# Performance work log

Hardware: AMD Instinct MI355X
Metric: run time of the kernel (lower is better)

Reference implementation:

```python
import jax, jax.numpy as jnp
import numpy as np

N_NODES = 100000
N_EDGES = 1600000
N_GRAPHS = 1024
F_NODE = 16
F_EDGE = 8
F_GRAPH = 10
F_OUT = 1
H = 64
EPS = 1e-7  # GENConv eps
T = 1.0     # GENConv softmax temperature (learn_t=False default)


def _lin_init(key, fi, fo):
    kw, kb = jax.random.split(key)
    s = 1.0 / np.sqrt(fi)
    W = jax.random.uniform(kw, (fi, fo), jnp.float32, -s, s)
    b = jax.random.uniform(kb, (fo,), jnp.float32, -s, s)
    return W, b


def setup_inputs() -> dict:
    key = jax.random.key(0)
    ks = jax.random.split(key, 24)
    inp = {
        'x': jax.random.normal(ks[0], (N_NODES, F_NODE), jnp.float32),
        'edge_attr': jax.random.normal(ks[1], (N_EDGES, F_EDGE), jnp.float32),
        'graph_attr': jax.random.normal(ks[2], (N_GRAPHS, F_GRAPH), jnp.float32),
        'edge_index': jax.random.randint(ks[3], (2, N_EDGES), 0, N_NODES),
        'batch': jnp.sort(jax.random.randint(ks[4], (N_NODES,), 0, N_GRAPHS)),
    }
    inp['node_W'], inp['node_b'] = _lin_init(ks[5], F_NODE, H)
    inp['edge_W'], inp['edge_b'] = _lin_init(ks[6], F_EDGE, H)
    # three GENConv MLPs: Linear(H,2H) -> BN(identity @eval) -> ReLU -> Linear(2H,H)
    for i, k1, k2 in ((1, ks[7], ks[8]), (2, ks[9], ks[10]), (3, ks[11], ks[12])):
        inp[f'c{i}_W1'], inp[f'c{i}_b1'] = _lin_init(k1, H, 2 * H)
        inp[f'c{i}_W2'], inp[f'c{i}_b2'] = _lin_init(k2, 2 * H, H)
    inp['d1_W'], inp['d1_b'] = _lin_init(ks[13], H + F_GRAPH, 32)
    inp['d2_W'], inp['d2_b'] = _lin_init(ks[14], 32, 32)
    inp['out_W'], inp['out_b'] = _lin_init(ks[15], 32, F_OUT)
    return inp


def _genconv(h, src, dst, ea, W1, b1, W2, b2):
    # message: relu(x_j + edge_attr) + eps   [E, H]
    msg = jax.nn.relu(h[src] + ea) + EPS
    # per-destination, per-feature segment softmax (aggr='softmax', t=1)
    m = jax.ops.segment_max(msg * T, dst, num_segments=N_NODES)   # [N, H]
    e = jnp.exp(msg * T - m[dst])                                  # [E, H]
    denom = jax.ops.segment_sum(e, dst, num_segments=N_NODES)     # [N, H]
    alpha = e / jnp.maximum(denom[dst], 1e-16)
    agg = jax.ops.segment_sum(msg * alpha, dst, num_segments=N_NODES)
    out = h + agg  # root add
    # MLP (BatchNorm is identity in eval with default stats)
    hid = jax.nn.relu(out @ W1 + b1)
    return hid @ W2 + b2


def reference(x, edge_attr, graph_attr, node_W, node_b, edge_W, edge_b,
              c1_W1, c1_b1, c1_W2, c1_b2,
              c2_W1, c2_b1, c2_W2, c2_b2,
              c3_W1, c3_b1, c3_W2, c3_b2,
              d1_W, d1_b, d2_W, d2_b, out_W, out_b,
              edge_index, batch):
    src, dst = edge_index[0], edge_index[1]
    h = x @ node_W + node_b
    ea = edge_attr @ edge_W + edge_b
    h = jax.nn.relu(_genconv(h, src, dst, ea, c1_W1, c1_b1, c1_W2, c1_b2))
    h = jax.nn.relu(_genconv(h, src, dst, ea, c2_W1, c2_b1, c2_W2, c2_b2))
    h = jax.nn.relu(_genconv(h, src, dst, ea, c3_W1, c3_b1, c3_W2, c3_b2))
    # global mean pool over graphs
    sums = jax.ops.segment_sum(h, batch, num_segments=N_GRAPHS)          # [G, H]
    cnt = jax.ops.segment_sum(jnp.ones((h.shape[0],), h.dtype), batch, num_segments=N_GRAPHS)
    pooled = sums / jnp.maximum(cnt, 1.0)[:, None]
    g = jnp.concatenate([pooled, graph_attr], axis=1)                    # [G, H+F_GRAPH]
    g = jax.nn.relu(g @ d1_W + d1_b)   # dropout = identity at eval
    g = jax.nn.relu(g @ d2_W + d2_b)
    return jax.nn.sigmoid(g @ out_W + out_b)                             # [G, 1]
```

## Files before the change

### kernel.cpp

```cpp
#include <hip/hip_runtime.h>
#include <hip/hip_bf16.h>

#define N_NODES 100000
#define N_EDGES 1600000
#define N_GRAPHS 1024
#define F_NODE 16
#define F_EDGE 8
#define F_GRAPH 10
#define HD 64
#define HD2 128
#define GEN_EPS 1e-7f
#define SCAN_NBLK ((N_NODES + 255) / 256)

typedef unsigned short u16;
typedef unsigned int u32;
typedef __attribute__((ext_vector_type(8))) short short8;
typedef __attribute__((ext_vector_type(4))) float floatx4;

__device__ __forceinline__ u16 f2bf(float x) {
    u32 u = __float_as_uint(x);
    return (u16)((u + 0x7FFFu + ((u >> 16) & 1u)) >> 16);
}
__device__ __forceinline__ float bf2f(u16 u) {
    return __uint_as_float(((u32)u) << 16);
}
__device__ __forceinline__ float u2f(unsigned int u) {
    return __uint_as_float(u);
}

__global__ void __launch_bounds__(256) k_node_embed(
        const float* __restrict__ x, const float* __restrict__ W,
        const float* __restrict__ b, float* __restrict__ h,
        u16* __restrict__ hb) {
    __shared__ float sW[F_NODE * HD];
    __shared__ float sb[HD];
    for (int i = threadIdx.x; i < F_NODE * HD; i += 256) sW[i] = W[i];
    if (threadIdx.x < HD) sb[threadIdx.x] = b[threadIdx.x];
    __syncthreads();
    int t = blockIdx.x * 256 + threadIdx.x;
    if (t >= N_NODES * HD) return;
    int n = t >> 6, f = t & 63;
    const float* xr = x + (size_t)n * F_NODE;
    float acc = sb[f];
#pragma unroll
    for (int k = 0; k < F_NODE; k++) acc += xr[k] * sW[k * HD + f];
    h[t] = acc;
    hb[t] = f2bf(acc);
}

__global__ void __launch_bounds__(256) k_hist(
        const int* __restrict__ dst, int* __restrict__ deg,
        int* __restrict__ rank) {
    int e = blockIdx.x * 256 + threadIdx.x;
    if (e >= N_EDGES) return;
    rank[e] = atomicAdd(&deg[dst[e]], 1);
}

__global__ void __launch_bounds__(256) k_scan1(
        const int* __restrict__ deg, int* __restrict__ bsum) {
    __shared__ int red[256];
    int t = threadIdx.x;
    int g = blockIdx.x * 256 + t;
    red[t] = (g < N_NODES) ? deg[g] : 0;
    __syncthreads();
    for (int s = 128; s > 0; s >>= 1) {
        if (t < s) red[t] += red[t + s];
        __syncthreads();
    }
    if (t == 0) bsum[blockIdx.x] = red[0];
}

__global__ void __launch_bounds__(512) k_scan2(
        const int* __restrict__ bsum, int* __restrict__ bpre) {
    __shared__ int sh[512];
    int t = threadIdx.x;
    int v = (t < SCAN_NBLK) ? bsum[t] : 0;
    sh[t] = v;
    __syncthreads();
    for (int d = 1; d < 512; d <<= 1) {
        int u = (t >= d) ? sh[t - d] : 0;
        __syncthreads();
        sh[t] += u;
        __syncthreads();
    }
    if (t < SCAN_NBLK) bpre[t] = sh[t] - v;
}

__global__ void __launch_bounds__(256) k_scan3(
        const int* __restrict__ deg, const int* __restrict__ bpre,
        int* __restrict__ off) {
    __shared__ int sh[256];
    int t = threadIdx.x;
    int g = blockIdx.x * 256 + t;
    int v = (g < N_NODES) ? deg[g] : 0;
    sh[t] = v;
    __syncthreads();
    for (int d = 1; d < 256; d <<= 1) {
        int u = (t >= d) ? sh[t - d] : 0;
        __syncthreads();
        sh[t] += u;
        __syncthreads();
    }
    int incl = sh[t];
    int base = bpre[blockIdx.x];
    if (g < N_NODES) off[g] = base + incl - v;
    if (g == N_NODES - 1) off[N_NODES] = base + incl;
}

__global__ void __launch_bounds__(256) k_scatter(
        const int* __restrict__ src, const int* __restrict__ dst,
        const int* __restrict__ rank, const int* __restrict__ off,
        const float* __restrict__ eattr,
        unsigned int* __restrict__ rec, int* __restrict__ srcs) {
    int e = blockIdx.x * 256 + threadIdx.x;
    if (e >= N_EDGES) return;
    const uint4* ap = reinterpret_cast<const uint4*>(eattr + (size_t)e * F_EDGE);
    uint4 a0 = ap[0], a1 = ap[1];
    int pos = off[dst[e]] + rank[e];
    uint4* op = reinterpret_cast<uint4*>(rec + (size_t)pos * 8);
    op[0] = a0;
    op[1] = a1;
    srcs[pos] = src[e];
}

__global__ void __launch_bounds__(256) k_gen_agg(
        const float* __restrict__ h, const u16* __restrict__ hb,
        const int* __restrict__ off,
        const unsigned int* __restrict__ rec,
        const int* __restrict__ srcs,
        const float* __restrict__ eW, const float* __restrict__ eb,
        float* __restrict__ outb) {
    int f = threadIdx.x & 63;
    float w[F_EDGE];
#pragma unroll
    for (int k = 0; k < F_EDGE; k++) w[k] = eW[k * HD + f];
    float bf = eb[f];
    int wave0 = blockIdx.x * 4 + (threadIdx.x >> 6);
    const int NW = gridDim.x * 4;
    for (int n0 = wave0; n0 < N_NODES; n0 += NW) {
        int n = __builtin_amdgcn_readfirstlane(n0);
        int beg = off[n], end = off[n + 1];
        size_t idx = (size_t)n * HD + f;
        float hroot = h[idx];
        float den = 0.f, nm = 0.f;
        int i = beg;
        for (; i + 8 <= end; i += 8) {
            uint4 q0[8], q1[8];
#pragma unroll
            for (int u = 0; u < 8; u++) {
                const uint4* rp = reinterpret_cast<const uint4*>(
                    rec + (size_t)(i + u) * 8);
                q0[u] = rp[0];
                q1[u] = rp[1];
            }
            int s[8];
#pragma unroll
            for (int u = 0; u < 8; u++) s[u] = srcs[i + u];
            float hv[8];
#pragma unroll
            for (int u = 0; u < 8; u++) hv[u] = bf2f(hb[(size_t)s[u] * HD + f]);
#pragma unroll
            for (int u = 0; u < 8; u++) {
                float ea = bf + u2f(q0[u].x) * w[0] + u2f(q0[u].y) * w[1]
                              + u2f(q0[u].z) * w[2] + u2f(q0[u].w) * w[3]
                              + u2f(q1[u].x) * w[4] + u2f(q1[u].y) * w[5]
                              + u2f(q1[u].z) * w[6] + u2f(q1[u].w) * w[7];
                float r = fmaxf(hv[u] + ea, 0.f);
                float ev = __expf(r);
                den += ev;
                nm += r * ev;
            }
        }
        for (; i < end; i++) {
            const uint4* rp = reinterpret_cast<const uint4*>(rec + (size_t)i * 8);
            uint4 q0 = rp[0], q1 = rp[1];
            int s = srcs[i];
            float hv = bf2f(hb[(size_t)s * HD + f]);
            float ea = bf + u2f(q0.x) * w[0] + u2f(q0.y) * w[1]
                          + u2f(q0.z) * w[2] + u2f(q0.w) * w[3]
                          + u2f(q1.x) * w[4] + u2f(q1.y) * w[5]
                          + u2f(q1.z) * w[6] + u2f(q1.w) * w[7];
            float r = fmaxf(hv + ea, 0.f);
            float ev = __expf(r);
            den += ev;
            nm += r * ev;
        }
        float agg = (end > beg) ? (nm / fmaxf(den, 1e-16f) + GEN_EPS) : 0.f;
        outb[idx] = hroot + agg;
    }
}

__global__ void __launch_bounds__(256) k_mlp(
        const float* __restrict__ inb,
        const float* __restrict__ W1, const float* __restrict__ b1,
        const float* __restrict__ W2, const float* __restrict__ b2,
        float* __restrict__ hout, u16* __restrict__ hbout) {
    __shared__ u16 wB1[HD2][HD + 8];
    __shared__ u16 wB2[HD][HD2 + 8];
    __shared__ u16 sHid[64][HD2 + 8];
    __shared__ float sb1[HD2];
    __shared__ float sb2[HD];
    int tid = threadIdx.x;
    for (int i = tid; i < HD * HD2; i += 256) {
        int f = i >> 7, j = i & 127;
        wB1[j][f] = f2bf(W1[i]);
    }
    for (int i = tid; i < HD2 * HD; i += 256) {
        int j = i >> 6, c = i & 63;
        wB2[c][j] = f2bf(W2[i]);
    }
    if (tid < HD2) sb1[tid] = b1[tid];
    if (tid < HD) sb2[tid] = b2[tid];
    __syncthreads();
    int wid = tid >> 6, lane = tid & 63;
    int quad = lane >> 4, lm = lane & 15;
    int n0 = blockIdx.x * 64 + wid * 16;
    bool active = (n0 < N_NODES);
    if (active) {
        int node = n0 + lm;
        short8 a[2];
        const float* ar = inb + (size_t)node * HD;
#pragma unroll
        for (int kk = 0; kk < 2; kk++) {
            const float4* p = reinterpret_cast<const float4*>(ar + kk * 32 + quad * 8);
            float4 v0 = p[0], v1 = p[1];
            short8 t;
            t[0] = (short)f2bf(v0.x); t[1] = (short)f2bf(v0.y);
            t[2] = (short)f2bf(v0.z); t[3] = (short)f2bf(v0.w);
            t[4] = (short)f2bf(v1.x); t[5] = (short)f2bf(v1.y);
            t[6] = (short)f2bf(v1.z); t[7] = (short)f2bf(v1.w);
            a[kk] = t;
        }
#pragma unroll
        for (int jt = 0; jt < 8; jt++) {
            int jb = jt * 16;
            float bias = sb1[jb + lm];
            floatx4 acc = {bias, bias, bias, bias};
#pragma unroll
            for (int kk = 0; kk < 2; kk++) {
                const short8* bp = reinterpret_cast<const short8*>(
                    &wB1[jb + lm][kk * 32 + quad * 8]);
                acc = __builtin_amdgcn_mfma_f32_16x16x32_bf16(a[kk], *bp, acc, 0, 0, 0);
            }
#pragma unroll
            for (int r = 0; r < 4; r++) {
                int lr = wid * 16 + quad * 4 + r;
                sHid[lr][jb + lm] = f2bf(fmaxf(acc[r], 0.f));
            }
        }
    }
    __syncthreads();
    if (active) {
        short8 a2[4];
#pragma unroll
        for (int kk = 0; kk < 4; kk++)
            a2[kk] = *reinterpret_cast<const short8*>(
                &sHid[wid * 16 + lm][kk * 32 + quad * 8]);
#pragma unroll
        for (int ct = 0; ct < 4; ct++) {
            int cb = ct * 16;
            float bias = sb2[cb + lm];
            floatx4 acc = {bias, bias, bias, bias};
#pragma unroll
            for (int kk = 0; kk < 4; kk++) {
                const short8* bp = reinterpret_cast<const short8*>(
                    &wB2[cb + lm][kk * 32 + quad * 8]);
                acc = __builtin_amdgcn_mfma_f32_16x16x32_bf16(a2[kk], *bp, acc, 0, 0, 0);
            }
#pragma unroll
            for (int r = 0; r < 4; r++) {
                int orow = n0 + quad * 4 + r;
                float o = fmaxf(acc[r], 0.f);
                hout[(size_t)orow * HD + cb + lm] = o;
                hbout[(size_t)orow * HD + cb + lm] = f2bf(o);
            }
        }
    }
}

__global__ void __launch_bounds__(256) k_pool(
        const float* __restrict__ h, const int* __restrict__ batch,
        float* __restrict__ pooled) {
    int g = blockIdx.x * 4 + (threadIdx.x >> 6);
    if (g >= N_GRAPHS) return;
    int f = threadIdx.x & 63;
    int lo = 0, hi = N_NODES;
    while (lo < hi) {
        int mid = (lo + hi) >> 1;
        if (batch[mid] < g) lo = mid + 1; else hi = mid;
    }
    int b = lo;
    int lo2 = b, hi2 = N_NODES;
    while (lo2 < hi2) {
        int mid = (lo2 + hi2) >> 1;
        if (batch[mid] < g + 1) lo2 = mid + 1; else hi2 = mid;
    }
    int e = lo2;
    float s = 0.f;
    for (int n = b; n < e; n++) s += h[(size_t)n * HD + f];
    float cnt = fmaxf((float)(e - b), 1.f);
    pooled[(size_t)g * HD + f] = s / cnt;
}

__global__ void __launch_bounds__(64) k_head(
        const float* __restrict__ pooled, const float* __restrict__ gattr,
        const float* __restrict__ d1W, const float* __restrict__ d1b,
        const float* __restrict__ d2W, const float* __restrict__ d2b,
        const float* __restrict__ oW, const float* __restrict__ ob,
        float* __restrict__ out) {
    int g = blockIdx.x;
    __shared__ float si[HD + F_GRAPH];
    __shared__ float s1[32], s2[32];
    int t = threadIdx.x;
    if (t < HD) si[t] = pooled[(size_t)g * HD + t];
    if (t < F_GRAPH) si[HD + t] = gattr[(size_t)g * F_GRAPH + t];
    __syncthreads();
    if (t < 32) {
        float acc = d1b[t];
        for (int i = 0; i < HD + F_GRAPH; i++) acc += si[i] * d1W[i * 32 + t];
        s1[t] = fmaxf(acc, 0.f);
    }
    __syncthreads();
    if (t < 32) {
        float acc = d2b[t];
        for (int i = 0; i < 32; i++) acc += s1[i] * d2W[i * 32 + t];
        s2[t] = fmaxf(acc, 0.f);
    }
    __syncthreads();
    if (t == 0) {
        float acc = ob[0];
        for (int i = 0; i < 32; i++) acc += s2[i] * oW[i];
        out[g] = 1.f / (1.f + __expf(-acc));
    }
}

extern "C" void kernel_launch(void* const* d_in, const int* in_sizes, int n_in,
                              void* d_out, int out_size, void* d_ws, size_t ws_size,
                              hipStream_t stream) {
    const float* x     = (const float*)d_in[0];
    const float* eattr = (const float*)d_in[1];
    const float* gattr = (const float*)d_in[2];
    const int*   eidx  = (const int*)d_in[3];
    const int*   batch = (const int*)d_in[4];
    const float* nodeW = (const float*)d_in[5];
    const float* nodeb = (const float*)d_in[6];
    const float* edgeW = (const float*)d_in[7];
    const float* edgeb = (const float*)d_in[8];
    const float* cW1[3] = {(const float*)d_in[9],  (const float*)d_in[13], (const float*)d_in[17]};
    const float* cb1[3] = {(const float*)d_in[10], (const float*)d_in[14], (const float*)d_in[18]};
    const float* cW2[3] = {(const float*)d_in[11], (const float*)d_in[15], (const float*)d_in[19]};
    const float* cb2[3] = {(const float*)d_in[12], (const float*)d_in[16], (const float*)d_in[20]};
    const float* d1W = (const float*)d_in[21];
    const float* d1b = (const float*)d_in[22];
    const float* d2W = (const float*)d_in[23];
    const float* d2b = (const float*)d_in[24];
    const float* oW  = (const float*)d_in[25];
    const float* ob  = (const float*)d_in[26];

    const int* src = eidx;
    const int* dst = eidx + N_EDGES;

    char* p = (char*)d_ws;
    float* h      = (float*)p; p += (size_t)N_NODES * HD * 4;
    float* outb   = (float*)p; p += (size_t)N_NODES * HD * 4;
    int*   srcs   = (int*)p;   p += (size_t)N_EDGES * 4;
    unsigned int* rec = (unsigned int*)p; p += (size_t)N_EDGES * F_EDGE * 4;
    u16*   hb     = (u16*)p;   p += (size_t)N_NODES * HD * 2;
    float* pooled = (float*)p; p += (size_t)N_GRAPHS * HD * 4;
    int*   off    = (int*)p;   p += (size_t)(N_NODES + 1) * 4;
    int*   deg    = (int*)p;   p += (size_t)N_NODES * 4;
    int*   rank   = (int*)p;   p += (size_t)N_EDGES * 4;
    int*   bsum   = (int*)p;   p += (size_t)(SCAN_NBLK + 1) * 4;
    int*   bpre   = (int*)p;   p += (size_t)(SCAN_NBLK + 1) * 4;

    const int EB = (N_EDGES + 255) / 256;
    const int NBM = (N_NODES + 63) / 64;

    k_node_embed<<<(N_NODES * HD + 255) / 256, 256, 0, stream>>>(x, nodeW, nodeb, h, hb);

    hipMemsetAsync(deg, 0, (size_t)N_NODES * 4, stream);
    k_hist<<<EB, 256, 0, stream>>>(dst, deg, rank);
    k_scan1<<<SCAN_NBLK, 256, 0, stream>>>(deg, bsum);
    k_scan2<<<1, 512, 0, stream>>>(bsum, bpre);
    k_scan3<<<SCAN_NBLK, 256, 0, stream>>>(deg, bpre, off);
    k_scatter<<<EB, 256, 0, stream>>>(src, dst, rank, off, eattr, rec, srcs);

    for (int l = 0; l < 3; l++) {
        k_gen_agg<<<2048, 256, 0, stream>>>(
            h, hb, off, rec, srcs, edgeW, edgeb, outb);
        k_mlp<<<NBM, 256, 0, stream>>>(outb, cW1[l], cb1[l], cW2[l], cb2[l], h, hb);
    }

    k_pool<<<(N_GRAPHS + 3) / 4, 256, 0, stream>>>(h, batch, pooled);
    k_head<<<N_GRAPHS, 64, 0, stream>>>(pooled, gattr,
                                        d1W, d1b, d2W, d2b, oW, ob,
                                        (float*)d_out);
}
```

Baseline: 716.7 us.

## Load edge records cooperatively per wave and broadcast via readlane; fuse hist with embed

In the aggregation kernel, each wave now loads 8 edge records (64 floats) with one coalesced per-lane load, plus 8 source indices, and broadcasts values with readlane. Previously every lane redundantly loaded the full 32-byte records. The next chunk is prefetched one step ahead, and the remainder loop is folded into a predicated main loop. The histogram and node-embedding kernels are merged into one launch, and edge buffers are padded by 8 entries so the over-read on the last chunk stays in bounds. In exchange, readlane adds scalar instruction overhead, and partial chunks run under per-edge predication.

Result: slower. 870.4 us (+21.4%).

```diff
diff --git a/kernel.cpp b/kernel.cpp
--- a/kernel.cpp
+++ b/kernel.cpp
@@ -11,6 +11,8 @@
 #define HD2 128
 #define GEN_EPS 1e-7f
 #define SCAN_NBLK ((N_NODES + 255) / 256)
+#define EB_BLK ((N_EDGES + 255) / 256)
+#define EMB_BLK ((N_NODES * HD + 255) / 256)
 
 typedef unsigned short u16;
 typedef unsigned int u32;
@@ -27,17 +29,28 @@
 __device__ __forceinline__ float u2f(unsigned int u) {
     return __uint_as_float(u);
 }
-
-__global__ void __launch_bounds__(256) k_node_embed(
+__device__ __forceinline__ float rlanef(u32 v, int l) {
+    return __uint_as_float((u32)__builtin_amdgcn_readlane((int)v, l));
+}
+
+__global__ void __launch_bounds__(256) k_front(
+        const int* __restrict__ dst, int* __restrict__ deg,
+        int* __restrict__ rank,
         const float* __restrict__ x, const float* __restrict__ W,
         const float* __restrict__ b, float* __restrict__ h,
         u16* __restrict__ hb) {
     __shared__ float sW[F_NODE * HD];
     __shared__ float sb[HD];
+    int bid = blockIdx.x;
+    if (bid < EB_BLK) {
+        int e = bid * 256 + threadIdx.x;
+        if (e < N_EDGES) rank[e] = atomicAdd(&deg[dst[e]], 1);
+        return;
+    }
     for (int i = threadIdx.x; i < F_NODE * HD; i += 256) sW[i] = W[i];
     if (threadIdx.x < HD) sb[threadIdx.x] = b[threadIdx.x];
     __syncthreads();
-    int t = blockIdx.x * 256 + threadIdx.x;
+    int t = (bid - EB_BLK) * 256 + threadIdx.x;
     if (t >= N_NODES * HD) return;
     int n = t >> 6, f = t & 63;
     const float* xr = x + (size_t)n * F_NODE;
@@ -46,14 +59,6 @@
     for (int k = 0; k < F_NODE; k++) acc += xr[k] * sW[k * HD + f];
     h[t] = acc;
     hb[t] = f2bf(acc);
-}
-
-__global__ void __launch_bounds__(256) k_hist(
-        const int* __restrict__ dst, int* __restrict__ deg,
-        int* __restrict__ rank) {
-    int e = blockIdx.x * 256 + threadIdx.x;
-    if (e >= N_EDGES) return;
-    rank[e] = atomicAdd(&deg[dst[e]], 1);
 }
 
 __global__ void __launch_bounds__(256) k_scan1(
@@ -130,7 +135,8 @@
         const int* __restrict__ srcs,
         const float* __restrict__ eW, const float* __restrict__ eb,
         float* __restrict__ outb) {
-    int f = threadIdx.x & 63;
+    int lane = threadIdx.x & 63;
+    int f = lane;
     float w[F_EDGE];
 #pragma unroll
     for (int k = 0; k < F_EDGE; k++) w[k] = eW[k * HD + f];
@@ -143,47 +149,44 @@
         size_t idx = (size_t)n * HD + f;
         float hroot = h[idx];
         float den = 0.f, nm = 0.f;
-        int i = beg;
-        for (; i + 8 <= end; i += 8) {
-            uint4 q0[8], q1[8];
-#pragma unroll
-            for (int u = 0; u < 8; u++) {
-                const uint4* rp = reinterpret_cast<const uint4*>(
-                    rec + (size_t)(i + u) * 8);
-                q0[u] = rp[0];
-                q1[u] = rp[1];
-            }
-            int s[8];
-#pragma unroll
-            for (int u = 0; u < 8; u++) s[u] = srcs[i + u];
-            float hv[8];
-#pragma unroll
-            for (int u = 0; u < 8; u++) hv[u] = bf2f(hb[(size_t)s[u] * HD + f]);
-#pragma unroll
-            for (int u = 0; u < 8; u++) {
-                float ea = bf + u2f(q0[u].x) * w[0] + u2f(q0[u].y) * w[1]
-                              + u2f(q0[u].z) * w[2] + u2f(q0[u].w) * w[3]
-                              + u2f(q1[u].x) * w[4] + u2f(q1[u].y) * w[5]
-                              + u2f(q1[u].z) * w[6] + u2f(q1[u].w) * w[7];
-                float r = fmaxf(hv[u] + ea, 0.f);
-                float ev = __expf(r);
-                den += ev;
-                nm += r * ev;
-            }
-        }
-        for (; i < end; i++) {
-            const uint4* rp = reinterpret_cast<const uint4*>(rec + (size_t)i * 8);
-            uint4 q0 = rp[0], q1 = rp[1];
-            int s = srcs[i];
-            float hv = bf2f(hb[(size_t)s * HD + f]);
-            float ea = bf + u2f(q0.x) * w[0] + u2f(q0.y) * w[1]
-                          + u2f(q0.z) * w[2] + u2f(q0.w) * w[3]
-                          + u2f(q1.x) * w[4] + u2f(q1.y) * w[5]
-                          + u2f(q1.z) * w[6] + u2f(q1.w) * w[7];
-            float r = fmaxf(hv + ea, 0.f);
-            float ev = __expf(r);
-            den += ev;
-            nm += r * ev;
+        if (beg < end) {
+            u32 bl = rec[(size_t)beg * 8 + lane];
+            int sv = srcs[beg + (lane & 7)];
+            for (int i = beg; i < end; i += 8) {
+                u32 blN = 0; int svN = 0;
+                int inx = i + 8;
+                if (inx < end) {
+                    blN = rec[(size_t)inx * 8 + lane];
+                    svN = srcs[inx + (lane & 7)];
+                }
+                float hv[8];
+#pragma unroll
+                for (int u = 0; u < 8; u++) {
+                    if (i + u < end) {
+                        int s = __builtin_amdgcn_readlane(sv, u);
+                        hv[u] = bf2f(hb[(size_t)s * HD + f]);
+                    }
+                }
+#pragma unroll
+                for (int u = 0; u < 8; u++) {
+                    if (i + u < end) {
+                        float ea = bf
+                            + rlanef(bl, 8 * u + 0) * w[0]
+                            + rlanef(bl, 8 * u + 1) * w[1]
+                            + rlanef(bl, 8 * u + 2) * w[2]
+                            + rlanef(bl, 8 * u + 3) * w[3]
+                            + rlanef(bl, 8 * u + 4) * w[4]
+                            + rlanef(bl, 8 * u + 5) * w[5]
+                            + rlanef(bl, 8 * u + 6) * w[6]
+                            + rlanef(bl, 8 * u + 7) * w[7];
+                        float r = fmaxf(hv[u] + ea, 0.f);
+                        float ev = __expf(r);
+                        den += ev;
+                        nm += r * ev;
+                    }
+                }
+                bl = blN; sv = svN;
+            }
         }
         float agg = (end > beg) ? (nm / fmaxf(den, 1e-16f) + GEN_EPS) : 0.f;
         outb[idx] = hroot + agg;
@@ -202,8 +205,8 @@
     __shared__ float sb2[HD];
     int tid = threadIdx.x;
     for (int i = tid; i < HD * HD2; i += 256) {
-        int f = i >> 7, j = i & 127;
-        wB1[j][f] = f2bf(W1[i]);
+        int ff = i >> 7, j = i & 127;
+        wB1[j][ff] = f2bf(W1[i]);
     }
     for (int i = tid; i < HD2 * HD; i += 256) {
         int j = i >> 6, c = i & 63;
@@ -363,8 +366,8 @@
     char* p = (char*)d_ws;
     float* h      = (float*)p; p += (size_t)N_NODES * HD * 4;
     float* outb   = (float*)p; p += (size_t)N_NODES * HD * 4;
-    int*   srcs   = (int*)p;   p += (size_t)N_EDGES * 4;
-    unsigned int* rec = (unsigned int*)p; p += (size_t)N_EDGES * F_EDGE * 4;
+    int*   srcs   = (int*)p;   p += (size_t)(N_EDGES + 8) * 4;
+    unsigned int* rec = (unsigned int*)p; p += (size_t)(N_EDGES + 8) * F_EDGE * 4;
     u16*   hb     = (u16*)p;   p += (size_t)N_NODES * HD * 2;
     float* pooled = (float*)p; p += (size_t)N_GRAPHS * HD * 4;
     int*   off    = (int*)p;   p += (size_t)(N_NODES + 1) * 4;
@@ -373,17 +376,15 @@
     int*   bsum   = (int*)p;   p += (size_t)(SCAN_NBLK + 1) * 4;
     int*   bpre   = (int*)p;   p += (size_t)(SCAN_NBLK + 1) * 4;
 
-    const int EB = (N_EDGES + 255) / 256;
     const int NBM = (N_NODES + 63) / 64;
 
-    k_node_embed<<<(N_NODES * HD + 255) / 256, 256, 0, stream>>>(x, nodeW, nodeb, h, hb);
-
     hipMemsetAsync(deg, 0, (size_t)N_NODES * 4, stream);
-    k_hist<<<EB, 256, 0, stream>>>(dst, deg, rank);
+    k_front<<<EB_BLK + EMB_BLK, 256, 0, stream>>>(dst, deg, rank,
+                                                  x, nodeW, nodeb, h, hb);
     k_scan1<<<SCAN_NBLK, 256, 0, stream>>>(deg, bsum);
     k_scan2<<<1, 512, 0, stream>>>(bsum, bpre);
     k_scan3<<<SCAN_NBLK, 256, 0, stream>>>(deg, bpre, off);
-    k_scatter<<<EB, 256, 0, stream>>>(src, dst, rank, off, eattr, rec, srcs);
+    k_scatter<<<EB_BLK, 256, 0, stream>>>(src, dst, rank, off, eattr, rec, srcs);
 
     for (int l = 0; l < 3; l++) {
         k_gen_agg<<<2048, 256, 0, stream>>>(
```

## Assign contiguous node chunks per wave and prefetch neighbor indices via lane broadcast

Applied to the files above, without the earlier changes.

Each wave now handles a contiguous range of KPW nodes instead of a strided set. It loads that range's offsets into lanes once and reads the per-node CSR bounds with readlane. Source indices for the next node are loaded one node ahead and broadcast lane-by-lane, so up to 32 neighbor feature gathers are issued before the edge-record loads. This removes dependent scalar loads of off and srcs from the inner loop. In exchange it adds padding of srcs and rec, a tail loop for nodes with degree above 32, and more register pressure from the 32-entry hv array.

Result: slower. 1.037 ms (+44.6%).

```diff
diff --git a/kernel.cpp b/kernel.cpp
--- a/kernel.cpp
+++ b/kernel.cpp
@@ -11,6 +11,9 @@
 #define HD2 128
 #define GEN_EPS 1e-7f
 #define SCAN_NBLK ((N_NODES + 255) / 256)
+#define AGG_BLK 2048
+#define NWAVES (AGG_BLK * 4)
+#define KPW ((N_NODES + NWAVES - 1) / NWAVES)
 
 typedef unsigned short u16;
 typedef unsigned int u32;
@@ -130,63 +133,94 @@
         const int* __restrict__ srcs,
         const float* __restrict__ eW, const float* __restrict__ eb,
         float* __restrict__ outb) {
-    int f = threadIdx.x & 63;
+    int lane = threadIdx.x & 63;
+    int f = lane;
     float w[F_EDGE];
 #pragma unroll
     for (int k = 0; k < F_EDGE; k++) w[k] = eW[k * HD + f];
     float bf = eb[f];
-    int wave0 = blockIdx.x * 4 + (threadIdx.x >> 6);
-    const int NW = gridDim.x * 4;
-    for (int n0 = wave0; n0 < N_NODES; n0 += NW) {
-        int n = __builtin_amdgcn_readfirstlane(n0);
-        int beg = off[n], end = off[n + 1];
-        size_t idx = (size_t)n * HD + f;
-        float hroot = h[idx];
+    int wv = blockIdx.x * 4 + (threadIdx.x >> 6);
+    int nbeg = wv * KPW;
+    if (nbeg >= N_NODES) return;
+    int nend = nbeg + KPW;
+    if (nend > N_NODES) nend = N_NODES;
+    int cnt = nend - nbeg;
+    int oidx = nbeg + lane;
+    if (oidx > N_NODES) oidx = N_NODES;
+    int offv = off[oidx];
+    int beg = __builtin_amdgcn_readlane(offv, 0);
+    int end = __builtin_amdgcn_readlane(offv, 1);
+    int sv = srcs[beg + lane];
+    float hroot = h[(size_t)nbeg * HD + f];
+    for (int j = 0; j < cnt; j++) {
+        int n = nbeg + j;
+        int deg = end - beg;
+        float hv[32];
+#pragma unroll
+        for (int g8 = 0; g8 < 4; g8++) {
+            if (g8 * 8 < deg) {
+#pragma unroll
+                for (int u = 0; u < 8; u++) {
+                    int s = __builtin_amdgcn_readlane(sv, g8 * 8 + u);
+                    hv[g8 * 8 + u] = bf2f(hb[(size_t)s * HD + f]);
+                }
+            }
+        }
+        int endN = 0, svN = 0;
+        float hrootN = 0.f;
+        if (j + 1 < cnt) {
+            endN = __builtin_amdgcn_readlane(offv, j + 2);
+            svN = srcs[end + lane];
+            hrootN = h[(size_t)(n + 1) * HD + f];
+        }
         float den = 0.f, nm = 0.f;
-        int i = beg;
-        for (; i + 8 <= end; i += 8) {
-            uint4 q0[8], q1[8];
-#pragma unroll
-            for (int u = 0; u < 8; u++) {
-                const uint4* rp = reinterpret_cast<const uint4*>(
-                    rec + (size_t)(i + u) * 8);
-                q0[u] = rp[0];
-                q1[u] = rp[1];
-            }
-            int s[8];
-#pragma unroll
-            for (int u = 0; u < 8; u++) s[u] = srcs[i + u];
-            float hv[8];
-#pragma unroll
-            for (int u = 0; u < 8; u++) hv[u] = bf2f(hb[(size_t)s[u] * HD + f]);
-#pragma unroll
-            for (int u = 0; u < 8; u++) {
-                float ea = bf + u2f(q0[u].x) * w[0] + u2f(q0[u].y) * w[1]
-                              + u2f(q0[u].z) * w[2] + u2f(q0[u].w) * w[3]
-                              + u2f(q1[u].x) * w[4] + u2f(q1[u].y) * w[5]
-                              + u2f(q1[u].z) * w[6] + u2f(q1[u].w) * w[7];
-                float r = fmaxf(hv[u] + ea, 0.f);
-                float ev = __expf(r);
-                den += ev;
-                nm += r * ev;
-            }
-        }
-        for (; i < end; i++) {
+#pragma unroll
+        for (int c = 0; c < 4; c++) {
+            int i0 = beg + c * 8;
+            if (i0 < end) {
+                uint4 q0[8], q1[8];
+#pragma unroll
+                for (int u = 0; u < 8; u++) {
+                    const uint4* rp = reinterpret_cast<const uint4*>(
+                        rec + (size_t)(i0 + u) * 8);
+                    q0[u] = rp[0];
+                    q1[u] = rp[1];
+                }
+#pragma unroll
+                for (int u = 0; u < 8; u++) {
+                    if (i0 + u < end) {
+                        float ea = bf + u2f(q0[u].x) * w[0] + u2f(q0[u].y) * w[1]
+                                      + u2f(q0[u].z) * w[2] + u2f(q0[u].w) * w[3]
+                                      + u2f(q1[u].x) * w[4] + u2f(q1[u].y) * w[5]
+                                      + u2f(q1[u].z) * w[6] + u2f(q1[u].w) * w[7];
+                        float r = fmaxf(hv[c * 8 + u] + ea, 0.f);
+                        float ev = __expf(r);
+                        den += ev;
+                        nm += r * ev;
+                    }
+                }
+            }
+        }
+        for (int i = beg + 32; i < end; i++) {
+            int s = srcs[i];
+            float hvv = bf2f(hb[(size_t)s * HD + f]);
             const uint4* rp = reinterpret_cast<const uint4*>(rec + (size_t)i * 8);
             uint4 q0 = rp[0], q1 = rp[1];
-            int s = srcs[i];
-            float hv = bf2f(hb[(size_t)s * HD + f]);
             float ea = bf + u2f(q0.x) * w[0] + u2f(q0.y) * w[1]
                           + u2f(q0.z) * w[2] + u2f(q0.w) * w[3]
                           + u2f(q1.x) * w[4] + u2f(q1.y) * w[5]
                           + u2f(q1.z) * w[6] + u2f(q1.w) * w[7];
-            float r = fmaxf(hv + ea, 0.f);
+            float r = fmaxf(hvv + ea, 0.f);
             float ev = __expf(r);
             den += ev;
             nm += r * ev;
         }
-        float agg = (end > beg) ? (nm / fmaxf(den, 1e-16f) + GEN_EPS) : 0.f;
-        outb[idx] = hroot + agg;
+        float agg = (deg > 0) ? (nm / fmaxf(den, 1e-16f) + GEN_EPS) : 0.f;
+        outb[(size_t)n * HD + f] = hroot + agg;
+        beg = end;
+        end = endN;
+        sv = svN;
+        hroot = hrootN;
     }
 }
 
@@ -202,8 +236,8 @@
     __shared__ float sb2[HD];
     int tid = threadIdx.x;
     for (int i = tid; i < HD * HD2; i += 256) {
-        int f = i >> 7, j = i & 127;
-        wB1[j][f] = f2bf(W1[i]);
+        int ff = i >> 7, j = i & 127;
+        wB1[j][ff] = f2bf(W1[i]);
     }
     for (int i = tid; i < HD2 * HD; i += 256) {
         int j = i >> 6, c = i & 63;
@@ -363,8 +397,8 @@
     char* p = (char*)d_ws;
     float* h      = (float*)p; p += (size_t)N_NODES * HD * 4;
     float* outb   = (float*)p; p += (size_t)N_NODES * HD * 4;
-    int*   srcs   = (int*)p;   p += (size_t)N_EDGES * 4;
-    unsigned int* rec = (unsigned int*)p; p += (size_t)N_EDGES * F_EDGE * 4;
+    int*   srcs   = (int*)p;   p += (size_t)(N_EDGES + 64) * 4;
+    unsigned int* rec = (unsigned int*)p; p += (size_t)(N_EDGES + 8) * F_EDGE * 4;
     u16*   hb     = (u16*)p;   p += (size_t)N_NODES * HD * 2;
     float* pooled = (float*)p; p += (size_t)N_GRAPHS * HD * 4;
     int*   off    = (int*)p;   p += (size_t)(N_NODES + 1) * 4;
@@ -379,6 +413,7 @@
     k_node_embed<<<(N_NODES * HD + 255) / 256, 256, 0, stream>>>(x, nodeW, nodeb, h, hb);
 
     hipMemsetAsync(deg, 0, (size_t)N_NODES * 4, stream);
+    hipMemsetAsync(srcs + N_EDGES, 0, 64 * sizeof(int), stream);
     k_hist<<<EB, 256, 0, stream>>>(dst, deg, rank);
     k_scan1<<<SCAN_NBLK, 256, 0, stream>>>(deg, bsum);
     k_scan2<<<1, 512, 0, stream>>>(bsum, bpre);
@@ -386,7 +421,7 @@
     k_scatter<<<EB, 256, 0, stream>>>(src, dst, rank, off, eattr, rec, srcs);
 
     for (int l = 0; l < 3; l++) {
-        k_gen_agg<<<2048, 256, 0, stream>>>(
+        k_gen_agg<<<AGG_BLK, 256, 0, stream>>>(
             h, hb, off, rec, srcs, edgeW, edgeb, outb);
         k_mlp<<<NBM, 256, 0, stream>>>(outb, cW1[l], cb1[l], cW2[l], cb2[l], h, hb);
     }
```

## Load edge attributes cooperatively per wave via LDS and prefetch next batch

Applied to the files above, without the earlier changes.

In the aggregation kernel, each wave now loads the 8 edges' attribute records with one coalesced 32-bit load per lane and shares them through shared memory. Previously every lane redundantly loaded all 64 bytes per edge. It also software-pipelines the loop, prefetching the next batch's source indices and attributes while the current batch's gathers and exps run. The tail loop is folded into masked batches, with padding added to the srcs/rec buffers so reads past the end stay in bounds. The cost is LDS traffic and implicit intra-wave synchronisation through shared memory.

Measured after the change: 698.9 us. -2.5%, faster.

```diff
diff --git a/kernel.cpp b/kernel.cpp
--- a/kernel.cpp
+++ b/kernel.cpp
@@ -130,12 +130,15 @@
         const int* __restrict__ srcs,
         const float* __restrict__ eW, const float* __restrict__ eb,
         float* __restrict__ outb) {
-    int f = threadIdx.x & 63;
+    __shared__ float sAttr[4][64];
+    int wid = threadIdx.x >> 6;
+    int lane = threadIdx.x & 63;
+    int f = lane;
     float w[F_EDGE];
 #pragma unroll
     for (int k = 0; k < F_EDGE; k++) w[k] = eW[k * HD + f];
     float bf = eb[f];
-    int wave0 = blockIdx.x * 4 + (threadIdx.x >> 6);
+    int wave0 = blockIdx.x * 4 + wid;
     const int NW = gridDim.x * 4;
     for (int n0 = wave0; n0 < N_NODES; n0 += NW) {
         int n = __builtin_amdgcn_readfirstlane(n0);
@@ -143,47 +146,54 @@
         size_t idx = (size_t)n * HD + f;
         float hroot = h[idx];
         float den = 0.f, nm = 0.f;
-        int i = beg;
-        for (; i + 8 <= end; i += 8) {
-            uint4 q0[8], q1[8];
-#pragma unroll
-            for (int u = 0; u < 8; u++) {
-                const uint4* rp = reinterpret_cast<const uint4*>(
-                    rec + (size_t)(i + u) * 8);
-                q0[u] = rp[0];
-                q1[u] = rp[1];
+        if (beg < end) {
+            int i = beg;
+            float av = 0.f;
+            if (beg + (lane >> 3) < end) av = u2f(rec[(size_t)beg * 8 + lane]);
+            int s8[8];
+#pragma unroll
+            for (int u = 0; u < 8; u++) s8[u] = srcs[beg + u];
+            while (true) {
+                float hv[8];
+#pragma unroll
+                for (int u = 0; u < 8; u++)
+                    hv[u] = bf2f(hb[(size_t)s8[u] * HD + f]);
+                int inx = i + 8;
+                bool more = inx < end;
+                float avN = 0.f;
+                int s8N[8];
+                if (more) {
+                    if (inx + (lane >> 3) < end)
+                        avN = u2f(rec[(size_t)inx * 8 + lane]);
+#pragma unroll
+                    for (int u = 0; u < 8; u++) s8N[u] = srcs[inx + u];
+                } else {
+#pragma unroll
+                    for (int u = 0; u < 8; u++) s8N[u] = 0;
+                }
+                sAttr[wid][lane] = av;
+#pragma unroll
+                for (int u = 0; u < 8; u++) {
+                    if (i + u < end) {
+                        const floatx4* A = reinterpret_cast<const floatx4*>(
+                            &sAttr[wid][u * 8]);
+                        floatx4 a0 = A[0], a1 = A[1];
+                        float ea = bf + a0.x * w[0] + a0.y * w[1]
+                                      + a0.z * w[2] + a0.w * w[3]
+                                      + a1.x * w[4] + a1.y * w[5]
+                                      + a1.z * w[6] + a1.w * w[7];
+                        float r = fmaxf(hv[u] + ea, 0.f);
+                        float ev = __expf(r);
+                        den += ev;
+                        nm += r * ev;
+                    }
+                }
+                if (!more) break;
+                i = inx;
+                av = avN;
+#pragma unroll
+                for (int u = 0; u < 8; u++) s8[u] = s8N[u];
             }
-            int s[8];
-#pragma unroll
-            for (int u = 0; u < 8; u++) s[u] = srcs[i + u];
-            float hv[8];
-#pragma unroll
-            for (int u = 0; u < 8; u++) hv[u] = bf2f(hb[(size_t)s[u] * HD + f]);
-#pragma unroll
-            for (int u = 0; u < 8; u++) {
-                float ea = bf + u2f(q0[u].x) * w[0] + u2f(q0[u].y) * w[1]
-                              + u2f(q0[u].z) * w[2] + u2f(q0[u].w) * w[3]
-                              + u2f(q1[u].x) * w[4] + u2f(q1[u].y) * w[5]
-                              + u2f(q1[u].z) * w[6] + u2f(q1[u].w) * w[7];
-                float r = fmaxf(hv[u] + ea, 0.f);
-                float ev = __expf(r);
-                den += ev;
-                nm += r * ev;
-            }
-        }
-        for (; i < end; i++) {
-            const uint4* rp = reinterpret_cast<const uint4*>(rec + (size_t)i * 8);
-            uint4 q0 = rp[0], q1 = rp[1];
-            int s = srcs[i];
-            float hv = bf2f(hb[(size_t)s * HD + f]);
-            float ea = bf + u2f(q0.x) * w[0] + u2f(q0.y) * w[1]
-                          + u2f(q0.z) * w[2] + u2f(q0.w) * w[3]
-                          + u2f(q1.x) * w[4] + u2f(q1.y) * w[5]
-                          + u2f(q1.z) * w[6] + u2f(q1.w) * w[7];
-            float r = fmaxf(hv + ea, 0.f);
-            float ev = __expf(r);
-            den += ev;
-            nm += r * ev;
         }
         float agg = (end > beg) ? (nm / fmaxf(den, 1e-16f) + GEN_EPS) : 0.f;
         outb[idx] = hroot + agg;
@@ -202,8 +212,8 @@
     __shared__ float sb2[HD];
     int tid = threadIdx.x;
     for (int i = tid; i < HD * HD2; i += 256) {
-        int f = i >> 7, j = i & 127;
-        wB1[j][f] = f2bf(W1[i]);
+        int ff = i >> 7, j = i & 127;
+        wB1[j][ff] = f2bf(W1[i]);
     }
     for (int i = tid; i < HD2 * HD; i += 256) {
         int j = i >> 6, c = i & 63;
@@ -363,8 +373,8 @@
     char* p = (char*)d_ws;
     float* h      = (float*)p; p += (size_t)N_NODES * HD * 4;
     float* outb   = (float*)p; p += (size_t)N_NODES * HD * 4;
-    int*   srcs   = (int*)p;   p += (size_t)N_EDGES * 4;
-    unsigned int* rec = (unsigned int*)p; p += (size_t)N_EDGES * F_EDGE * 4;
+    int*   srcs   = (int*)p;   p += (size_t)(N_EDGES + 64) * 4;
+    unsigned int* rec = (unsigned int*)p; p += (size_t)(N_EDGES + 8) * F_EDGE * 4;
     u16*   hb     = (u16*)p;   p += (size_t)N_NODES * HD * 2;
     float* pooled = (float*)p; p += (size_t)N_GRAPHS * HD * 4;
     int*   off    = (int*)p;   p += (size_t)(N_NODES + 1) * 4;
@@ -379,6 +389,7 @@
     k_node_embed<<<(N_NODES * HD + 255) / 256, 256, 0, stream>>>(x, nodeW, nodeb, h, hb);
 
     hipMemsetAsync(deg, 0, (size_t)N_NODES * 4, stream);
+    hipMemsetAsync(srcs + N_EDGES, 0, 64 * sizeof(int), stream);
     k_hist<<<EB, 256, 0, stream>>>(dst, deg, rank);
     k_scan1<<<SCAN_NBLK, 256, 0, stream>>>(deg, bsum);
     k_scan2<<<1, 512, 0, stream>>>(bsum, bpre);
```
